# Optimization experiments

Measured on AMD Instinct MI355X. Metric: run time of the kernel, lower is better.

## Reference

```python
import jax, jax.numpy as jnp
import numpy as np

ALPHA = 0.2   # LeakyReLU slope from source
HEADS = 8

def _proj(x, W, s, b):
    # Conv3D(kernel=1, no bias) + fused inference BatchNorm affine + LeakyReLU
    y = jnp.einsum('nchwd,de->nchwe', x, W) * s + b
    return jnp.where(y >= 0, y, ALPHA * y)

def setup_inputs() -> dict:
    key = jax.random.key(0)
    ks = jax.random.split(key, 13)
    N, D, H, W, C = 2, 64, 64, 64, 64   # D == in_channels (axis 1), C is last axis
    KC, VC = 64, 64
    p = lambda k, sh, sc=0.1: jax.random.normal(k, sh, jnp.float32) * sc
    return {
        'x':  jax.random.normal(ks[0], (N, D, H, W, C), jnp.float32),
        'Wk': p(ks[1], (D, KC)), 'sk': 1.0 + p(ks[2], (KC,)), 'bk': p(ks[3], (KC,)),
        'Wq': p(ks[4], (D, KC)), 'sq': 1.0 + p(ks[5], (KC,)), 'bq': p(ks[6], (KC,)),
        'Wv': p(ks[7], (D, VC)), 'sv': 1.0 + p(ks[8], (VC,)), 'bv': p(ks[9], (VC,)),
        'Wr': p(ks[10], (VC, D)), 'sr': 1.0 + p(ks[11], (D,)), 'br': p(ks[12], (D,)),
    }

def reference(x, Wk, sk, bk, Wq, sq, bq, Wv, sv, bv, Wr, sr, br):
    n, d, h, w, c = x.shape
    xt = jnp.transpose(x, (0, 4, 2, 3, 1))            # (n, c, h, w, d)
    keys    = _proj(xt, Wk, sk, bk)                   # (n, c, h, w, KC)
    queries = _proj(xt, Wq, sq, bq)
    values  = _proj(xt, Wv, sv, bv)
    T = c * h * w
    KC, VC = Wk.shape[1], Wv.shape[1]
    hk, hv = KC // HEADS, VC // HEADS                 # hk == hv required by source math
    K = jax.nn.softmax(keys.reshape(n, T, HEADS, hk), axis=1)      # softmax over tokens
    Q = jax.nn.softmax(queries.reshape(n, T, HEADS, hk), axis=-1)  # softmax over head channels
    V = values.reshape(n, T, HEADS, hv)
    ctx = jnp.einsum('ntak,ntav->nakv', K, V)         # (n, heads, hk, hv) small context
    # source: tf.matmul(context, query^T) contracts ctx's hv with query's hk axis
    att = jnp.einsum('nakv,ntav->nakt', ctx, Q)       # (n, heads, hk, T)
    # faithful raw reshape per head (n, hk, T) -> (n, c, h, w, hv), heads concat last
    att = att.reshape(n, HEADS, c, h, w, hv)
    agg = jnp.transpose(att, (0, 2, 3, 4, 1, 5)).reshape(n, c, h, w, HEADS * hv)
    rep = _proj(agg, Wr, sr, br)                      # (n, c, h, w, d)
    return x + jnp.transpose(rep, (0, 4, 2, 3, 1))
```

## Files before the change

kernel.cpp:

```cpp
#include <hip/hip_runtime.h>

#define ALPHA 0.2f

typedef const __attribute__((address_space(1))) unsigned int gu32;
typedef __attribute__((address_space(3))) unsigned int lu32;

__device__ float g_part[8192 * 576];
__device__ float g_red[2 * 32 * 1024];
__device__ float g_ctx[1024];

__global__ __launch_bounds__(256) void k_kv(
    const float* __restrict__ x,
    const float* __restrict__ Wk, const float* __restrict__ sk, const float* __restrict__ bk,
    const float* __restrict__ Wv, const float* __restrict__ sv, const float* __restrict__ bv)
{
  __shared__ __align__(16) float sh[11008];
  float* eK = sh;
  float* vV = sh + 4352;
  float* pE = sh + 8704;
  float* pS = sh + 8960;

  const int tid = threadIdx.x;
  const int bid = blockIdx.x;
  const int n   = bid >> 11;
  const int hw0 = (bid & 2047) * 2;

  const int pr  = tid & 63;
  const int wv  = __builtin_amdgcn_readfirstlane(tid >> 6);
  const bool isK = (wv < 2);
  const int cbase = 32 * (wv & 1);
  const float* Wsrc = (isK ? Wk : Wv) + cbase;
  const float* sp   = (isK ? sk : sv) + cbase;
  const float* bp   = (isK ? bk : bv) + cbase;

  const float* xg = x + (size_t)n * 16777216u + (size_t)hw0 * 64u + 2 * pr;

  float acc[2][32];
  #pragma unroll
  for (int t = 0; t < 2; ++t)
    #pragma unroll
    for (int c = 0; c < 32; ++c) acc[t][c] = 0.f;

  #pragma unroll 4
  for (int d = 0; d < 64; ++d) {
    float2 xv = *(const float2*)(xg + (size_t)d * 262144u);
    const float* wrow = Wsrc + d * 64;
    #pragma unroll
    for (int q = 0; q < 8; ++q) {
      float4 w = *(const float4*)(wrow + q * 4);
      acc[0][q*4+0] += xv.x * w.x; acc[0][q*4+1] += xv.x * w.y;
      acc[0][q*4+2] += xv.x * w.z; acc[0][q*4+3] += xv.x * w.w;
      acc[1][q*4+0] += xv.y * w.x; acc[1][q*4+1] += xv.y * w.y;
      acc[1][q*4+2] += xv.y * w.z; acc[1][q*4+3] += xv.y * w.w;
    }
  }

  #pragma unroll
  for (int q = 0; q < 8; ++q) {
    float4 s4 = *(const float4*)(sp + q * 4);
    float4 b4 = *(const float4*)(bp + q * 4);
    float ss[4] = {s4.x, s4.y, s4.z, s4.w};
    float bb[4] = {b4.x, b4.y, b4.z, b4.w};
    #pragma unroll
    for (int j = 0; j < 4; ++j) {
      #pragma unroll
      for (int t = 0; t < 2; ++t) {
        float y = acc[t][q*4+j] * ss[j] + bb[j];
        y = (y >= 0.f) ? y : ALPHA * y;
        if (isK) y = __expf(fminf(y, 60.f));
        acc[t][q*4+j] = y;
      }
    }
  }

  const int prl = pr & 31;
  float* dstbuf = isK ? eK : vV;
  const int ch = tid & 63, tq = tid >> 6, a8 = ch & ~7;

  #pragma unroll
  for (int ph = 0; ph < 2; ++ph) {
    if ((pr >> 5) == ph) {
      #pragma unroll
      for (int t = 0; t < 2; ++t)
        #pragma unroll
        for (int q = 0; q < 8; ++q)
          *(float4*)&dstbuf[(prl*2 + t) * 68 + cbase + q*4] = *(float4*)&acc[t][q*4];
    }
    __syncthreads();

    float E = 0.f;
    float S[8];
    #pragma unroll
    for (int v = 0; v < 8; ++v) S[v] = 0.f;
    for (int t = tq * 16; t < tq * 16 + 16; ++t) {
      float e = eK[t * 68 + ch];
      float4 v0 = *(const float4*)&vV[t * 68 + a8];
      float4 v1 = *(const float4*)&vV[t * 68 + a8 + 4];
      E += e;
      S[0] += e * v0.x; S[1] += e * v0.y; S[2] += e * v0.z; S[3] += e * v0.w;
      S[4] += e * v1.x; S[5] += e * v1.y; S[6] += e * v1.z; S[7] += e * v1.w;
    }
    pE[tq * 64 + ch] = E;
    #pragma unroll
    for (int v = 0; v < 8; ++v) pS[(tq * 64 + ch) * 8 + v] = S[v];
    __syncthreads();

    if (tid < 64) {
      float* gp = g_part + ((size_t)bid * 2u + ph) * 576u;
      float E4 = pE[tid] + pE[64 + tid] + pE[128 + tid] + pE[192 + tid];
      gp[tid] = E4;
      #pragma unroll
      for (int v = 0; v < 8; ++v) {
        float S4 = pS[tid * 8 + v] + pS[(64 + tid) * 8 + v]
                 + pS[(128 + tid) * 8 + v] + pS[(192 + tid) * 8 + v];
        gp[64 + v * 64 + tid] = S4;
      }
    }
  }
}

__global__ __launch_bounds__(256) void k_red() {
  const int ob = blockIdx.x & 3;
  const int bc = blockIdx.x >> 2;
  const int i  = ob * 256 + threadIdx.x;
  const int n = i >> 9, ch = (i & 511) >> 3, v = i & 7;
  const float* base = g_part + ((size_t)n * 4096u + (size_t)bc * 128u) * 576u;
  float l = 0.f, S = 0.f;
  #pragma unroll 8
  for (int b = 0; b < 128; ++b) {
    l += base[(size_t)b * 576u + ch];
    S += base[(size_t)b * 576u + 64u + (size_t)v * 64u + ch];
  }
  g_red[bc * 1024 + i]         = l;
  g_red[32768 + bc * 1024 + i] = S;
}

__global__ __launch_bounds__(256) void k_ctx() {
  int i = blockIdx.x * 256 + threadIdx.x;
  if (i >= 1024) return;
  float l = 0.f, S = 0.f;
  #pragma unroll
  for (int r = 0; r < 32; ++r) {
    l += g_red[r * 1024 + i];
    S += g_red[32768 + r * 1024 + i];
  }
  float c = (l > 0.f) ? (S / l) : 0.f;
  if (!(__builtin_fabsf(c) < 1e30f)) c = 0.f;
  g_ctx[i] = c;
}

__global__ __launch_bounds__(256) void k_att(
    const float* __restrict__ x,
    const float* __restrict__ Wq, const float* __restrict__ sq, const float* __restrict__ bq,
    const float* __restrict__ Wr, const float* __restrict__ sr, const float* __restrict__ br,
    float* __restrict__ out)
{
  __shared__ __align__(16) float WqA[64 * 68];
  __shared__ __align__(16) float xw[64 * 64];
  __shared__ __align__(16) float qL[64 * 64];
  __shared__ __align__(16) float ctxL[64 * 12];
  __shared__ float srL[64], brL[64];

  const int tid = threadIdx.x;
  const int lin = blockIdx.x;

  const int xcd   = lin & 7;
  const int jc    = (lin >> 3) & 7;
  const int rest  = lin >> 6;
  const int combo = rest * 8 + xcd;
  const int n     = combo >> 9;
  const int hp_lo = (combo >> 6) & 7;
  const int wp    = combo & 63;
  const int hp    = jc * 8 + hp_lo;
  const int hwp   = hp * 64 + wp;

  const int h_t   = hp_lo * 8 + (wp >> 3);
  const int wbase = (wp & 7) * 8;

  #pragma unroll
  for (int i = 0; i < 4; ++i) {
    int idx = tid + i * 256;
    __builtin_amdgcn_global_load_lds((gu32*)(Wq + idx * 4),
                                     (lu32*)&WqA[idx * 4], 16, 0, 0);
  }
  if (tid < 64) { srL[tid] = sr[tid]; brL[tid] = br[tid]; }

  for (int i = tid; i < 512; i += 256) {
    int ch = i >> 3, v = i & 7;
    ctxL[ch * 12 + v] = g_ctx[n * 512 + ch * 8 + v];
  }

  {
    const size_t xb = (size_t)n * 16777216u + (size_t)h_t * 4096u;
    #pragma unroll
    for (int i = 0; i < 16; ++i) {
      int idx = tid + i * 256;
      int d = idx >> 6, tok = idx & 63;
      int vpp = tok >> 3, cl = tok & 7;
      xw[d * 64 + tok] = x[xb + (size_t)d * 262144u + (size_t)(wbase + vpp) * 64u + (cl * 8 + jc)];
    }
  }
  __syncthreads();

  {
    const int tok0 = (tid & 31) * 2;
    const int ch0  = (tid >> 5) * 8;
    float acc0[8], acc1[8];
    #pragma unroll
    for (int j = 0; j < 8; ++j) { acc0[j] = 0.f; acc1[j] = 0.f; }
    #pragma unroll 4
    for (int d = 0; d < 64; ++d) {
      float2 xv = *(const float2*)&xw[d * 64 + tok0];
      float4 wa = *(const float4*)&WqA[d * 64 + ch0];
      float4 wb = *(const float4*)&WqA[d * 64 + ch0 + 4];
      float w[8] = {wa.x, wa.y, wa.z, wa.w, wb.x, wb.y, wb.z, wb.w};
      #pragma unroll
      for (int j = 0; j < 8; ++j) { acc0[j] += xv.x * w[j]; acc1[j] += xv.y * w[j]; }
    }
    float sv8[8], bv8[8];
    *(float4*)&sv8[0] = *(const float4*)(sq + ch0);
    *(float4*)&sv8[4] = *(const float4*)(sq + ch0 + 4);
    *(float4*)&bv8[0] = *(const float4*)(bq + ch0);
    *(float4*)&bv8[4] = *(const float4*)(bq + ch0 + 4);
    #pragma unroll
    for (int i = 0; i < 2; ++i) {
      float* a = (i == 0) ? acc0 : acc1;
      float mx = -3.0e38f;
      #pragma unroll
      for (int j = 0; j < 8; ++j) {
        float y = a[j] * sv8[j] + bv8[j];
        y = (y >= 0.f) ? y : ALPHA * y;
        a[j] = y;
        mx = fmaxf(mx, y);
      }
      float sum = 0.f;
      #pragma unroll
      for (int j = 0; j < 8; ++j) { a[j] = __expf(a[j] - mx); sum += a[j]; }
      float inv = 1.f / sum;
      float o8[8];
      #pragma unroll
      for (int j = 0; j < 8; ++j) o8[j] = a[j] * inv;
      const int t = tok0 + i;
      const int rot = (4 * t) & 63;
      *(float4*)&qL[t * 64 + ((ch0 + rot) & 63)]     = *(float4*)&o8[0];
      *(float4*)&qL[t * 64 + ((ch0 + 4 + rot) & 63)] = *(float4*)&o8[4];
    }
  }
  __syncthreads();

  {
    float* aggL = WqA;
    const int cp = tid & 63, eb = tid >> 6;
    const int kk = cp >> 3, cl = cp & 7;
    #pragma unroll
    for (int j4 = 0; j4 < 4; ++j4) {
      float s4[4];
      #pragma unroll
      for (int jj = 0; jj < 4; ++jj) {
        int e = eb * 16 + j4 * 4 + jj;
        int a = e >> 3, vpp = e & 7;
        float4 c0 = *(const float4*)&ctxL[(a * 8 + kk) * 12];
        float4 c1 = *(const float4*)&ctxL[(a * 8 + kk) * 12 + 4];
        int t = vpp * 8 + cl;
        int rot = (4 * t) & 63;
        float4 q0 = *(const float4*)&qL[t * 64 + ((a * 8 + rot) & 63)];
        float4 q1 = *(const float4*)&qL[t * 64 + ((a * 8 + 4 + rot) & 63)];
        s4[jj] = q0.x * c0.x + q0.y * c0.y + q0.z * c0.z + q0.w * c0.w
               + q1.x * c1.x + q1.y * c1.y + q1.z * c1.z + q1.w * c1.w;
      }
      *(float4*)&aggL[cp * 68 + eb * 16 + j4 * 4] =
          make_float4(s4[0], s4[1], s4[2], s4[3]);
    }
  }
  __syncthreads();

  {
    const float* aggL = WqA;
    const int ci = tid & 63, dq = tid >> 6;
    const int dqu = __builtin_amdgcn_readfirstlane(tid >> 6);
    const float* WrU = Wr + dqu * 16;
    float accr[16];
    #pragma unroll
    for (int i = 0; i < 16; ++i) accr[i] = 0.f;
    #pragma unroll 4
    for (int ec = 0; ec < 16; ++ec) {
      float4 a4 = *(const float4*)&aggL[ci * 68 + ec * 4];
      float av[4] = {a4.x, a4.y, a4.z, a4.w};
      #pragma unroll
      for (int j = 0; j < 4; ++j) {
        const float* wrow = WrU + (ec * 4 + j) * 64;
        float4 w0 = *(const float4*)(wrow);
        float4 w1 = *(const float4*)(wrow + 4);
        float4 w2 = *(const float4*)(wrow + 8);
        float4 w3 = *(const float4*)(wrow + 12);
        float aj = av[j];
        accr[0]  += aj * w0.x; accr[1]  += aj * w0.y; accr[2]  += aj * w0.z; accr[3]  += aj * w0.w;
        accr[4]  += aj * w1.x; accr[5]  += aj * w1.y; accr[6]  += aj * w1.z; accr[7]  += aj * w1.w;
        accr[8]  += aj * w2.x; accr[9]  += aj * w2.y; accr[10] += aj * w2.z; accr[11] += aj * w2.w;
        accr[12] += aj * w3.x; accr[13] += aj * w3.y; accr[14] += aj * w3.z; accr[15] += aj * w3.w;
      }
    }
    const size_t xb = (size_t)n * 16777216u + (size_t)hwp * 64u + (size_t)ci;
    #pragma unroll
    for (int i = 0; i < 16; ++i) {
      int di = dq * 16 + i;
      float y = accr[i] * srL[di] + brL[di];
      y = (y >= 0.f) ? y : ALPHA * y;
      out[xb + (size_t)di * 262144u] = x[xb + (size_t)di * 262144u] + y;
    }
  }
}

extern "C" void kernel_launch(void* const* d_in, const int* in_sizes, int n_in,
                              void* d_out, int out_size, void* d_ws, size_t ws_size,
                              hipStream_t stream)
{
  (void)in_sizes; (void)n_in; (void)out_size; (void)d_ws; (void)ws_size;

  const float* x  = (const float*)d_in[0];
  const float* Wk = (const float*)d_in[1];
  const float* sk = (const float*)d_in[2];
  const float* bk = (const float*)d_in[3];
  const float* Wq = (const float*)d_in[4];
  const float* sq = (const float*)d_in[5];
  const float* bq = (const float*)d_in[6];
  const float* Wv = (const float*)d_in[7];
  const float* sv = (const float*)d_in[8];
  const float* bv = (const float*)d_in[9];
  const float* Wr = (const float*)d_in[10];
  const float* sr = (const float*)d_in[11];
  const float* br = (const float*)d_in[12];
  float* out = (float*)d_out;

  k_kv  <<<dim3(4096), dim3(256), 0, stream>>>(x, Wk, sk, bk, Wv, sv, bv);
  k_red <<<dim3(128),  dim3(256), 0, stream>>>();
  k_ctx <<<dim3(4),    dim3(256), 0, stream>>>();
  k_att <<<dim3(8192), dim3(256), 0, stream>>>(x, Wq, sq, bq, Wr, sr, br, out);
}
```

Measured before the change: 523.4 us.

## Stage projection weights in LDS via async loads and widen reduction grid

k_kv now copies Wk and Wv into shared memory with global_load_lds and reads weight rows from LDS instead of scalar/global loads, with scale/bias hoisted into registers before the loop. k_att likewise stages Wr into LDS, overlapping the copy with the aggregation step. The pS partial-sum layout is transposed to avoid bank conflicts, and k_red doubles its grid to 256 blocks with half the blocks per reduction. These changes trade uniform scalar loads for LDS traffic and extra syncs, and k_ctx now sums twice as many partials.

```diff
diff --git a/kernel.cpp b/kernel.cpp
--- a/kernel.cpp
+++ b/kernel.cpp
@@ -6,7 +6,7 @@
 typedef __attribute__((address_space(3))) unsigned int lu32;
 
 __device__ float g_part[8192 * 576];
-__device__ float g_red[2 * 32 * 1024];
+__device__ float g_red[2 * 64 * 1024];
 __device__ float g_ctx[1024];
 
 __global__ __launch_bounds__(256) void k_kv(
@@ -15,6 +15,7 @@
     const float* __restrict__ Wv, const float* __restrict__ sv, const float* __restrict__ bv)
 {
   __shared__ __align__(16) float sh[11008];
+  float* W2 = sh;
   float* eK = sh;
   float* vV = sh + 4352;
   float* pE = sh + 8704;
@@ -25,13 +26,28 @@
   const int n   = bid >> 11;
   const int hw0 = (bid & 2047) * 2;
 
+  #pragma unroll
+  for (int i = 0; i < 8; ++i) {
+    int idx = tid + i * 256;
+    int d = idx >> 5, e4 = (idx & 31) * 4;
+    const float* src = (e4 < 64) ? (Wk + d * 64 + e4) : (Wv + d * 64 + e4 - 64);
+    __builtin_amdgcn_global_load_lds((gu32*)src, (lu32*)&W2[idx * 4], 16, 0, 0);
+  }
+
   const int pr  = tid & 63;
-  const int wv  = __builtin_amdgcn_readfirstlane(tid >> 6);
+  const int wv  = tid >> 6;
   const bool isK = (wv < 2);
   const int cbase = 32 * (wv & 1);
-  const float* Wsrc = (isK ? Wk : Wv) + cbase;
-  const float* sp   = (isK ? sk : sv) + cbase;
-  const float* bp   = (isK ? bk : bv) + cbase;
+  const int wcol  = wv * 32;
+  const float* sp = (isK ? sk : sv) + cbase;
+  const float* bp = (isK ? bk : bv) + cbase;
+
+  float s8a[8][4], b8a[8][4];
+  #pragma unroll
+  for (int q = 0; q < 8; ++q) {
+    *(float4*)&s8a[q][0] = *(const float4*)(sp + q * 4);
+    *(float4*)&b8a[q][0] = *(const float4*)(bp + q * 4);
+  }
 
   const float* xg = x + (size_t)n * 16777216u + (size_t)hw0 * 64u + 2 * pr;
 
@@ -41,10 +57,12 @@
     #pragma unroll
     for (int c = 0; c < 32; ++c) acc[t][c] = 0.f;
 
-  #pragma unroll 4
+  __syncthreads();
+
+  #pragma unroll 2
   for (int d = 0; d < 64; ++d) {
     float2 xv = *(const float2*)(xg + (size_t)d * 262144u);
-    const float* wrow = Wsrc + d * 64;
+    const float* wrow = &W2[d * 128 + wcol];
     #pragma unroll
     for (int q = 0; q < 8; ++q) {
       float4 w = *(const float4*)(wrow + q * 4);
@@ -57,21 +75,19 @@
 
   #pragma unroll
   for (int q = 0; q < 8; ++q) {
-    float4 s4 = *(const float4*)(sp + q * 4);
-    float4 b4 = *(const float4*)(bp + q * 4);
-    float ss[4] = {s4.x, s4.y, s4.z, s4.w};
-    float bb[4] = {b4.x, b4.y, b4.z, b4.w};
     #pragma unroll
     for (int j = 0; j < 4; ++j) {
       #pragma unroll
       for (int t = 0; t < 2; ++t) {
-        float y = acc[t][q*4+j] * ss[j] + bb[j];
+        float y = acc[t][q*4+j] * s8a[q][j] + b8a[q][j];
         y = (y >= 0.f) ? y : ALPHA * y;
         if (isK) y = __expf(fminf(y, 60.f));
         acc[t][q*4+j] = y;
       }
     }
   }
+
+  __syncthreads();
 
   const int prl = pr & 31;
   float* dstbuf = isK ? eK : vV;
@@ -102,7 +118,7 @@
     }
     pE[tq * 64 + ch] = E;
     #pragma unroll
-    for (int v = 0; v < 8; ++v) pS[(tq * 64 + ch) * 8 + v] = S[v];
+    for (int v = 0; v < 8; ++v) pS[v * 256 + tq * 64 + ch] = S[v];
     __syncthreads();
 
     if (tid < 64) {
@@ -111,8 +127,8 @@
       gp[tid] = E4;
       #pragma unroll
       for (int v = 0; v < 8; ++v) {
-        float S4 = pS[tid * 8 + v] + pS[(64 + tid) * 8 + v]
-                 + pS[(128 + tid) * 8 + v] + pS[(192 + tid) * 8 + v];
+        float S4 = pS[v * 256 + tid] + pS[v * 256 + 64 + tid]
+                 + pS[v * 256 + 128 + tid] + pS[v * 256 + 192 + tid];
         gp[64 + v * 64 + tid] = S4;
       }
     }
@@ -124,15 +140,15 @@
   const int bc = blockIdx.x >> 2;
   const int i  = ob * 256 + threadIdx.x;
   const int n = i >> 9, ch = (i & 511) >> 3, v = i & 7;
-  const float* base = g_part + ((size_t)n * 4096u + (size_t)bc * 128u) * 576u;
+  const float* base = g_part + ((size_t)n * 4096u + (size_t)bc * 64u) * 576u;
   float l = 0.f, S = 0.f;
   #pragma unroll 8
-  for (int b = 0; b < 128; ++b) {
+  for (int b = 0; b < 64; ++b) {
     l += base[(size_t)b * 576u + ch];
     S += base[(size_t)b * 576u + 64u + (size_t)v * 64u + ch];
   }
   g_red[bc * 1024 + i]         = l;
-  g_red[32768 + bc * 1024 + i] = S;
+  g_red[65536 + bc * 1024 + i] = S;
 }
 
 __global__ __launch_bounds__(256) void k_ctx() {
@@ -140,9 +156,9 @@
   if (i >= 1024) return;
   float l = 0.f, S = 0.f;
   #pragma unroll
-  for (int r = 0; r < 32; ++r) {
+  for (int r = 0; r < 64; ++r) {
     l += g_red[r * 1024 + i];
-    S += g_red[32768 + r * 1024 + i];
+    S += g_red[65536 + r * 1024 + i];
   }
   float c = (l > 0.f) ? (S / l) : 0.f;
   if (!(__builtin_fabsf(c) < 1e30f)) c = 0.f;
@@ -248,6 +264,13 @@
   }
   __syncthreads();
 
+  #pragma unroll
+  for (int i = 0; i < 4; ++i) {
+    int idx = tid + i * 256;
+    __builtin_amdgcn_global_load_lds((gu32*)(Wr + idx * 4),
+                                     (lu32*)&xw[idx * 4], 16, 0, 0);
+  }
+
   {
     float* aggL = WqA;
     const int cp = tid & 63, eb = tid >> 6;
@@ -277,8 +300,6 @@
   {
     const float* aggL = WqA;
     const int ci = tid & 63, dq = tid >> 6;
-    const int dqu = __builtin_amdgcn_readfirstlane(tid >> 6);
-    const float* WrU = Wr + dqu * 16;
     float accr[16];
     #pragma unroll
     for (int i = 0; i < 16; ++i) accr[i] = 0.f;
@@ -288,7 +309,7 @@
       float av[4] = {a4.x, a4.y, a4.z, a4.w};
       #pragma unroll
       for (int j = 0; j < 4; ++j) {
-        const float* wrow = WrU + (ec * 4 + j) * 64;
+        const float* wrow = &xw[(ec * 4 + j) * 64 + dq * 16];
         float4 w0 = *(const float4*)(wrow);
         float4 w1 = *(const float4*)(wrow + 4);
         float4 w2 = *(const float4*)(wrow + 8);
@@ -333,7 +354,7 @@
   float* out = (float*)d_out;
 
   k_kv  <<<dim3(4096), dim3(256), 0, stream>>>(x, Wk, sk, bk, Wv, sv, bv);
-  k_red <<<dim3(128),  dim3(256), 0, stream>>>();
+  k_red <<<dim3(256),  dim3(256), 0, stream>>>();
   k_ctx <<<dim3(4),    dim3(256), 0, stream>>>();
   k_att <<<dim3(8192), dim3(256), 0, stream>>>(x, Wq, sq, bq, Wr, sr, br, out);
 }
```

Result: slower. 640.6 us (+22.4%).
